# Performance work log

Hardware: AMD Instinct MI355X
Metric: run time of the kernel (lower is better)

The kernel has to match this reference:

```python
import jax, jax.numpy as jnp
import numpy as np

EMB = 1024
HEADS = 16
QKV = 64
INNER = 2816  # 256 * ceil(2*1024*4/3 / 256)


def rms_norm(x, w, eps=1e-6):
    xf = x.astype(jnp.float32)
    n = xf * jax.lax.rsqrt(jnp.mean(xf * xf, axis=-1, keepdims=True) + eps)
    return n.astype(x.dtype) * w


def setup_inputs() -> dict:
    key = jax.random.key(0)
    ks = jax.random.split(key, 12)
    s = 0.02
    return {
        "x": jax.random.normal(ks[0], (4, 2048, EMB), dtype=jnp.float32),
        "Wq": jax.random.normal(ks[1], (HEADS * QKV, EMB), dtype=jnp.float32) * s,
        "Wk": jax.random.normal(ks[2], (HEADS * QKV, EMB), dtype=jnp.float32) * s,
        "Wv": jax.random.normal(ks[3], (HEADS * QKV, EMB), dtype=jnp.float32) * s,
        "Wc": jax.random.normal(ks[4], (EMB, HEADS * QKV), dtype=jnp.float32) * s,
        "bc": jnp.zeros((EMB,), dtype=jnp.float32),
        "g1": jnp.ones((EMB,), dtype=jnp.float32),
        "g2": jnp.ones((EMB,), dtype=jnp.float32),
        "L1": jax.random.normal(ks[5], (INNER, EMB), dtype=jnp.float32) * s,
        "L2": jax.random.normal(ks[6], (INNER, EMB), dtype=jnp.float32) * s,
        "L3": jax.random.normal(ks[7], (EMB, INNER), dtype=jnp.float32) * s,
    }


def reference(x, Wq, Wk, Wv, Wc, bc, g1, g2, L1, L2, L3):
    B, N, D = x.shape
    # QKV projections (torch Linear: y = x @ W.T), split into heads: [B,H,N,dk]
    q = (x @ Wq.T).reshape(B, N, HEADS, QKV).transpose(0, 2, 1, 3)
    k = (x @ Wk.T).reshape(B, N, HEADS, QKV).transpose(0, 2, 1, 3)
    v = (x @ Wv.T).reshape(B, N, HEADS, QKV).transpose(0, 2, 1, 3)
    # attention: explicit score matrix [B,H,N,N]
    score = jnp.einsum("bhnd,bhmd->bhnm", q, k) / jnp.sqrt(jnp.float32(QKV))
    weights = jax.nn.softmax(score, axis=-1)
    out = jnp.einsum("bhnm,bhmd->bhnd", weights, v)
    out = out.transpose(0, 2, 1, 3).reshape(B, N, HEADS * QKV)
    mha = out @ Wc.T + bc
    h = rms_norm(x + mha, g1)
    # parallel gated MLP: silu(h@L1.T) * (h@L2.T) @ L3.T
    ff = (jax.nn.silu(h @ L1.T) * (h @ L2.T)) @ L3.T
    return rms_norm(h + ff, g2)
```

## Files before the change

### kernel.cpp

```cpp
#include <hip/hip_runtime.h>
#include <hip/hip_bf16.h>


#define EMB   1024
#define HEADS 16
#define DK    64
#define INNER 2816
#define BATCH 4
#define NTOK  2048
#define MROWS (BATCH * NTOK)

#define QSCALE 0.18033688011112042f

typedef short bf16x8 __attribute__((ext_vector_type(8)));
typedef short s16x4  __attribute__((ext_vector_type(4)));
typedef float f32x4  __attribute__((ext_vector_type(4)));

typedef const void __attribute__((address_space(1)))* gas_cvp;
typedef void       __attribute__((address_space(3)))* las_vp;

__device__ __forceinline__ short to_bf16(float f) {
  union { float f; unsigned u; } x; x.f = f;
  unsigned r = x.u + 0x7FFFu + ((x.u >> 16) & 1u);
  return (short)(r >> 16);
}

__device__ __forceinline__ unsigned cvt_pk_bf16(float a, float b) {
  unsigned r;
  asm("v_cvt_pk_bf16_f32 %0, %1, %2" : "=v"(r) : "v"(a), "v"(b));
  return r;
}

__device__ __forceinline__ void gld16(void* lds, const void* g) {
  __builtin_amdgcn_global_load_lds((gas_cvp)g, (las_vp)lds, 16, 0, 0);
}

__global__ __launch_bounds__(256, 4)
void cvtk(const float* __restrict__ s, short* __restrict__ d, int n4) {
  int i = blockIdx.x * 256 + threadIdx.x;
  if (i < n4) {
    float4 v = ((const float4*)s)[i];
    s16x4 o;
    o[0] = to_bf16(v.x); o[1] = to_bf16(v.y);
    o[2] = to_bf16(v.z); o[3] = to_bf16(v.w);
    ((s16x4*)d)[i] = o;
  }
}

__global__ __launch_bounds__(256, 4)
void cvt_inter(const float* __restrict__ L1, const float* __restrict__ L2,
               short* __restrict__ d) {
  int i = blockIdx.x * 256 + threadIdx.x;
  if (i >= INNER * 256) return;
  int row = i >> 8, c4 = i & 255;
  float4 v1 = ((const float4*)L1)[i];
  float4 v2 = ((const float4*)L2)[i];
  s16x4 o1, o2;
  o1[0]=to_bf16(v1.x); o1[1]=to_bf16(v1.y); o1[2]=to_bf16(v1.z); o1[3]=to_bf16(v1.w);
  o2[0]=to_bf16(v2.x); o2[1]=to_bf16(v2.y); o2[2]=to_bf16(v2.z); o2[3]=to_bf16(v2.w);
  ((s16x4*)d)[(size_t)(2 * row) * 256 + c4]     = o1;
  ((s16x4*)d)[(size_t)(2 * row + 1) * 256 + c4] = o2;
}

template<int MODE>
__global__ __launch_bounds__(256, 2)
void gemm_bt(const short* __restrict__ A, const short* __restrict__ Bw,
             int M, int N, int K,
             void* __restrict__ out0,
             const float* __restrict__ aux0, const float* __restrict__ aux1)
{
  __shared__ short At[128 * 64];
  __shared__ short Bt[128 * 64];
  const int t = threadIdx.x;
  const int lane = t & 63;
  const int l15 = lane & 15, lhi = lane >> 4;
  const int w  = t >> 6;
  const int wm = (w >> 1) << 6;
  const int wn = (w & 1) << 6;
  const int tilesN = N >> 7;
  const int m0 = (blockIdx.x / tilesN) << 7;
  const int n0 = (blockIdx.x % tilesN) << 7;

  const int r = t >> 3;
  const int p = t & 7;
  const int psrc = p ^ (r & 7);
  const short* Ag = A  + (size_t)(m0 + r) * K + psrc * 8;
  const short* Bg = Bw + (size_t)(n0 + r) * K + psrc * 8;

  f32x4 acc[4][4];
  const f32x4 fz = {0.f, 0.f, 0.f, 0.f};
#pragma unroll
  for (int i = 0; i < 4; i++)
#pragma unroll
    for (int j = 0; j < 4; j++) acc[i][j] = fz;

  int aoff[2][4], boff[2][4];
#pragma unroll
  for (int kk = 0; kk < 2; kk++)
#pragma unroll
    for (int mt = 0; mt < 4; mt++) {
      int ra = wm + mt * 16 + l15;
      aoff[kk][mt] = ra * 128 + ((kk * 64 + lhi * 16) ^ ((ra & 7) << 4));
      int rb = wn + mt * 16 + l15;
      boff[kk][mt] = rb * 128 + ((kk * 64 + lhi * 16) ^ ((rb & 7) << 4));
    }

  for (int k0 = 0; k0 < K; k0 += 64) {
#pragma unroll
    for (int i = 0; i < 4; i++) {
      gld16((char*)At + t * 16 + i * 4096, Ag + (size_t)i * 32 * K + k0);
      gld16((char*)Bt + t * 16 + i * 4096, Bg + (size_t)i * 32 * K + k0);
    }
    __syncthreads();
#pragma unroll
    for (int kk = 0; kk < 2; kk++) {
      bf16x8 a[4], b[4];
#pragma unroll
      for (int mt = 0; mt < 4; mt++)
        a[mt] = *(const bf16x8*)((const char*)At + aoff[kk][mt]);
#pragma unroll
      for (int nt = 0; nt < 4; nt++)
        b[nt] = *(const bf16x8*)((const char*)Bt + boff[kk][nt]);
#pragma unroll
      for (int mt = 0; mt < 4; mt++)
#pragma unroll
        for (int nt = 0; nt < 4; nt++)
          acc[mt][nt] = __builtin_amdgcn_mfma_f32_16x16x32_bf16(
              a[mt], b[nt], acc[mt][nt], 0, 0, 0);
    }
    __syncthreads();
  }

#pragma unroll
  for (int mt = 0; mt < 4; mt++) {
#pragma unroll
    for (int nt = 0; nt < 4; nt++) {
      const int mb = m0 + wm + mt * 16 + lhi * 4;
      const int n  = n0 + wn + nt * 16 + l15;
      if constexpr (MODE == 1) {
#pragma unroll
        for (int j = 0; j < 4; j++) {
          size_t idx = (size_t)(mb + j) * 1024 + n;
          ((float*)out0)[idx] = acc[mt][nt][j] + aux1[n] + aux0[idx];
        }
      } else {
#pragma unroll
        for (int j = 0; j < 4; j++) {
          size_t idx = (size_t)(mb + j) * 1024 + n;
          ((float*)out0)[idx] = acc[mt][nt][j] + aux0[idx];
        }
      }
    }
  }
}

#define G256_LDA(buf, mh) do {                                              \
  const char* _b = (const char*)&lds[buf][0][0] + (mh) * 8192;              \
  _Pragma("unroll") for (int mt = 0; mt < 4; mt++)                          \
    _Pragma("unroll") for (int kk = 0; kk < 2; kk++)                        \
      af[mt][kk] = *(const bf16x8*)(_b + aoff[mt][kk]);                     \
} while (0)

#define G256_LDB(buf, nh) do {                                              \
  const char* _b = (const char*)&lds[buf][1][0] + (nh) * 4096;              \
  _Pragma("unroll") for (int nt = 0; nt < 2; nt++)                          \
    _Pragma("unroll") for (int kk = 0; kk < 2; kk++)                        \
      bN[nh][nt][kk] = *(const bf16x8*)(_b + boff[nt][kk]);                 \
} while (0)

#define G256_MFQ(mh, nh) do {                                               \
  __builtin_amdgcn_s_setprio(1);                                            \
  _Pragma("unroll") for (int mt = 0; mt < 4; mt++)                          \
    _Pragma("unroll") for (int nt = 0; nt < 2; nt++)                        \
      _Pragma("unroll") for (int kk = 0; kk < 2; kk++)                      \
        acc[(mh)*4+mt][(nh)*2+nt] = __builtin_amdgcn_mfma_f32_16x16x32_bf16(\
            af[mt][kk], bN[nh][nt][kk], acc[(mh)*4+mt][(nh)*2+nt], 0, 0, 0);\
  __builtin_amdgcn_s_setprio(0);                                            \
} while (0)

#define G256_SYNC() do {                                                    \
  __builtin_amdgcn_s_barrier();                                             \
  asm volatile("s_waitcnt lgkmcnt(0)" ::: "memory");                        \
  __builtin_amdgcn_sched_barrier(0);                                        \
} while (0)

template<int MODE>
__global__ __launch_bounds__(512, 2)
void gemm256(const short* __restrict__ A, const short* __restrict__ Bw,
             int M, int N, int K,
             void* __restrict__ out0, void* __restrict__ out1,
             void* __restrict__ out2)
{
  __shared__ short lds[2][2][16384];
  const int t = threadIdx.x;
  const int lane = t & 63;
  const int l15 = lane & 15, lhi = lane >> 4;
  const int w = t >> 6;
  const int wr = w >> 2, wc = w & 3;

  const int chunk = gridDim.x >> 3;
  const int bid = blockIdx.x;
  const int wg = (bid & 7) * chunk + (bid >> 3);
  const int tilesM = M >> 8;
  const int m0 = (wg % tilesM) << 8;
  const int n0 = (wg / tilesM) << 8;

  const int r = t >> 3, p = t & 7;
  const int psrc = p ^ (r & 7);
  const short* Ag = A  + (size_t)(m0 + r) * K + psrc * 8;
  const short* Bg = Bw + (size_t)(n0 + r) * K + psrc * 8;
  const int NT = K >> 6;

  f32x4 acc[8][4];
  const f32x4 fz = {0.f, 0.f, 0.f, 0.f};
#pragma unroll
  for (int i = 0; i < 8; i++)
#pragma unroll
    for (int j = 0; j < 4; j++) acc[i][j] = fz;

  int aoff[4][2], boff[2][2];
#pragma unroll
  for (int mt = 0; mt < 4; mt++)
#pragma unroll
    for (int kk = 0; kk < 2; kk++)
      aoff[mt][kk] = (wr * 128 + mt * 16 + l15) * 128 +
                     ((kk * 64 + lhi * 16) ^ ((l15 & 7) << 4));
#pragma unroll
  for (int nt = 0; nt < 2; nt++)
#pragma unroll
    for (int kk = 0; kk < 2; kk++)
      boff[nt][kk] = (wc * 64 + nt * 16 + l15) * 128 +
                     ((kk * 64 + lhi * 16) ^ ((l15 & 7) << 4));

  bf16x8 af[4][2], bN[2][2][2];

  auto stg = [&](int buf, int kt, int hh) {
    const int sel = hh >> 1, hf = hh & 1;
    short* dst = &lds[buf][sel][hf * 8192] + t * 8;
    const short* src = (sel ? Bg : Ag) + (size_t)(hf * 128) * K + kt * 64;
    gld16(dst, src);
    gld16(dst + 4096, src + (size_t)64 * K);
  };

  stg(0, 0, 0); stg(0, 0, 1); stg(0, 0, 2); stg(0, 0, 3);
  stg(1, 1, 0);
  asm volatile("s_waitcnt vmcnt(2)" ::: "memory");
  __builtin_amdgcn_s_barrier();

  for (int i = 0; i < NT / 2; ++i) {
    const int T1 = 2 * i + 1, T2 = 2 * i + 2, T3 = 2 * i + 3;
    G256_LDA(0, 0); G256_LDB(0, 0);
    stg(1, T1, 1);
    G256_SYNC();
    G256_MFQ(0, 0);
    __builtin_amdgcn_s_barrier();
    G256_LDB(0, 1);
    stg(1, T1, 2);
    G256_SYNC();
    G256_MFQ(0, 1);
    __builtin_amdgcn_s_barrier();
    G256_LDA(0, 1);
    stg(1, T1, 3);
    G256_SYNC();
    G256_MFQ(1, 1);
    __builtin_amdgcn_s_barrier();
    if (T2 < NT) stg(0, T2, 0);
    G256_SYNC();
    G256_MFQ(1, 0);
    if (T2 < NT) asm volatile("s_waitcnt vmcnt(2)" ::: "memory");
    else         asm volatile("s_waitcnt vmcnt(0)" ::: "memory");
    __builtin_amdgcn_s_barrier();
    G256_LDA(1, 0); G256_LDB(1, 0);
    if (T2 < NT) stg(0, T2, 1);
    G256_SYNC();
    G256_MFQ(0, 0);
    __builtin_amdgcn_s_barrier();
    G256_LDB(1, 1);
    if (T2 < NT) stg(0, T2, 2);
    G256_SYNC();
    G256_MFQ(0, 1);
    __builtin_amdgcn_s_barrier();
    G256_LDA(1, 1);
    if (T2 < NT) stg(0, T2, 3);
    G256_SYNC();
    G256_MFQ(1, 1);
    __builtin_amdgcn_s_barrier();
    if (T3 < NT) stg(1, T3, 0);
    G256_SYNC();
    G256_MFQ(1, 0);
    if (T3 < NT) asm volatile("s_waitcnt vmcnt(2)" ::: "memory");
    else         asm volatile("s_waitcnt vmcnt(0)" ::: "memory");
    __builtin_amdgcn_s_barrier();
  }

#pragma unroll
  for (int mt = 0; mt < 8; mt++) {
#pragma unroll
    for (int nt = 0; nt < 4; nt++) {
      const int mb = m0 + wr * 128 + mt * 16 + lhi * 4;
      const int n  = n0 + wc * 64 + nt * 16 + l15;
      if constexpr (MODE == 0) {
        const int which = n >> 10, c = n & 1023;
        if (which == 2) {
          const int hh = c >> 6, dd = c & 63;
          const int bb = mb >> 11, tok = mb & 2047;
          s16x4 pk;
#pragma unroll
          for (int j = 0; j < 4; j++) pk[j] = to_bf16(acc[mt][nt][j]);
          *(s16x4*)((short*)out2 +
                    (size_t)((bb * HEADS + hh) * DK + dd) * NTOK + tok) = pk;
        } else {
          short* dst = (which == 0) ? (short*)out0 : (short*)out1;
          const float scl = (which == 0) ? QSCALE : 1.0f;
#pragma unroll
          for (int j = 0; j < 4; j++)
            dst[(size_t)(mb + j) * 1024 + c] = to_bf16(acc[mt][nt][j] * scl);
        }
      } else {
#pragma unroll
        for (int j = 0; j < 4; j++) {
          float v0 = acc[mt][nt][j];
          float v1 = __shfl_xor(v0, 1);
          if ((lane & 1) == 0) {
            float su = v0 / (1.f + __expf(-v0));
            ((short*)out0)[(size_t)(mb + j) * INNER + (n >> 1)] =
                to_bf16(su * v1);
          }
        }
      }
    }
  }
}

__global__ __launch_bounds__(256, 3)
void attn_k(const short* __restrict__ qb, const short* __restrict__ kb,
            const short* __restrict__ vtb, short* __restrict__ ob)
{
  __shared__ short Kt[2][64 * 64];
  __shared__ short Vt[2][64 * 64];
  __shared__ short Pt[128 * 68];
  const int t = threadIdx.x;
  const int lane = t & 63;
  const int l15 = lane & 15, lhi = lane >> 4;
  const int w = t >> 6;
  const int bh = blockIdx.x;
  const int b = bh >> 4, h = bh & 15;
  const int q0 = blockIdx.y << 7;

  bf16x8 aq[2][2];
#pragma unroll
  for (int s = 0; s < 2; s++) {
    const short* qp = qb + (size_t)(b * NTOK + q0 + w * 32 + s * 16 + l15) * EMB
                         + h * DK + lhi * 8;
    aq[s][0] = *(const bf16x8*)qp;
    aq[s][1] = *(const bf16x8*)(qp + 32);
  }

  f32x4 acc[2][4];
  const f32x4 fz = {0.f, 0.f, 0.f, 0.f};
#pragma unroll
  for (int s = 0; s < 2; s++)
#pragma unroll
    for (int dt = 0; dt < 4; dt++) acc[s][dt] = fz;
  float m_run[2] = {-1e30f, -1e30f};
  float l_run[2] = {0.f, 0.f};

  const int r = t >> 3, p = t & 7;
  const int psrc = p ^ (r & 7);
  const short* kg = kb  + (size_t)(b * NTOK + r) * EMB + h * DK + psrc * 8;
  const short* vg = vtb + (size_t)(bh * DK + r) * NTOK + psrc * 8;

  int kvoff[4][2];
#pragma unroll
  for (int x = 0; x < 4; x++)
#pragma unroll
    for (int kk = 0; kk < 2; kk++) {
      int row = x * 16 + l15;
      kvoff[x][kk] = row * 128 + ((kk * 64 + lhi * 16) ^ ((row & 7) << 4));
    }
  int pw[2][4], pr[2][2];
#pragma unroll
  for (int s = 0; s < 2; s++) {
    const int prow = w * 32 + s * 16 + l15;
#pragma unroll
    for (int kvt = 0; kvt < 4; kvt++) pw[s][kvt] = prow * 136 + kvt * 32 + lhi * 8;
#pragma unroll
    for (int kk = 0; kk < 2; kk++)   pr[s][kk]  = prow * 136 + kk * 64 + lhi * 16;
  }

  auto stage = [&](short* Kd, short* Vd, int kv0) {
    const short* ks = kg + (size_t)kv0 * EMB;
    const short* vs = vg + kv0;
    gld16(Kd + t * 8,        ks);
    gld16(Kd + t * 8 + 2048, ks + (size_t)32 * EMB);
    gld16(Vd + t * 8,        vs);
    gld16(Vd + t * 8 + 2048, vs + (size_t)32 * NTOK);
  };

  auto do_set = [&](f32x4 (&sv)[4], float& mr, float& lr, f32x4 (&ac)[4],
                    const int (&pwo)[4]) {
    float pm = sv[0][0];
#pragma unroll
    for (int kvt = 0; kvt < 4; kvt++)
#pragma unroll
      for (int j = 0; j < 4; j++) pm = fmaxf(pm, sv[kvt][j]);
    if (__any(pm > mr + 8.0f)) {
      pm = fmaxf(pm, __shfl_xor(pm, 16));
      pm = fmaxf(pm, __shfl_xor(pm, 32));
      const float mnew = fmaxf(mr, pm);
      const float al = exp2f(mr - mnew);
      lr *= al;
#pragma unroll
      for (int dt = 0; dt < 4; dt++)
#pragma unroll
        for (int j = 0; j < 4; j++) ac[dt][j] *= al;
      mr = mnew;
    }
    float ls = 0.f;
#pragma unroll
    for (int kvt = 0; kvt < 4; kvt++)
#pragma unroll
      for (int j = 0; j < 4; j++) {
        float pe = exp2f(sv[kvt][j] - mr);
        sv[kvt][j] = pe;
        ls += pe;
      }
    lr += ls;
#pragma unroll
    for (int kvt = 0; kvt < 4; kvt++) {
      uint2 u;
      u.x = cvt_pk_bf16(sv[kvt][0], sv[kvt][1]);
      u.y = cvt_pk_bf16(sv[kvt][2], sv[kvt][3]);
      *(uint2*)((char*)Pt + pwo[kvt]) = u;
    }
  };

  auto compute = [&](const short* Kb_, const short* Vb_) {
    const char* Kb = (const char*)Kb_;
    const char* Vb = (const char*)Vb_;
    bf16x8 kf[4][2];
#pragma unroll
    for (int x = 0; x < 4; x++)
#pragma unroll
      for (int kk = 0; kk < 2; kk++)
        kf[x][kk] = *(const bf16x8*)(Kb + kvoff[x][kk]);
    f32x4 s0[4], s1[4];
    __builtin_amdgcn_s_setprio(1);
#pragma unroll
    for (int kvt = 0; kvt < 4; kvt++) {
      s0[kvt] = __builtin_amdgcn_mfma_f32_16x16x32_bf16(kf[kvt][0], aq[0][0], fz, 0, 0, 0);
      s0[kvt] = __builtin_amdgcn_mfma_f32_16x16x32_bf16(kf[kvt][1], aq[0][1], s0[kvt], 0, 0, 0);
      s1[kvt] = __builtin_amdgcn_mfma_f32_16x16x32_bf16(kf[kvt][0], aq[1][0], fz, 0, 0, 0);
      s1[kvt] = __builtin_amdgcn_mfma_f32_16x16x32_bf16(kf[kvt][1], aq[1][1], s1[kvt], 0, 0, 0);
    }
    __builtin_amdgcn_s_setprio(0);
    do_set(s0, m_run[0], l_run[0], acc[0], pw[0]);
    do_set(s1, m_run[1], l_run[1], acc[1], pw[1]);
    bf16x8 vf[4][2];
#pragma unroll
    for (int dt = 0; dt < 4; dt++)
#pragma unroll
      for (int kk = 0; kk < 2; kk++)
        vf[dt][kk] = *(const bf16x8*)(Vb + kvoff[dt][kk]);
    bf16x8 pb0[2], pb1[2];
#pragma unroll
    for (int kk = 0; kk < 2; kk++) {
      pb0[kk] = *(const bf16x8*)((const char*)Pt + pr[0][kk]);
      pb1[kk] = *(const bf16x8*)((const char*)Pt + pr[1][kk]);
    }
    __builtin_amdgcn_s_setprio(1);
#pragma unroll
    for (int dt = 0; dt < 4; dt++) {
#pragma unroll
      for (int kk = 0; kk < 2; kk++)
        acc[0][dt] = __builtin_amdgcn_mfma_f32_16x16x32_bf16(vf[dt][kk], pb0[kk], acc[0][dt], 0, 0, 0);
#pragma unroll
      for (int kk = 0; kk < 2; kk++)
        acc[1][dt] = __builtin_amdgcn_mfma_f32_16x16x32_bf16(vf[dt][kk], pb1[kk], acc[1][dt], 0, 0, 0);
    }
    __builtin_amdgcn_s_setprio(0);
  };

  stage(Kt[0], Vt[0], 0);
  for (int it = 0; it < 32; it += 2) {
    stage(Kt[1], Vt[1], (it + 1) * 64);
    asm volatile("s_waitcnt vmcnt(4)" ::: "memory");
    __builtin_amdgcn_s_barrier();
    compute(Kt[0], Vt[0]);
    __builtin_amdgcn_s_barrier();
    if (it + 2 < 32) {
      stage(Kt[0], Vt[0], (it + 2) * 64);
      asm volatile("s_waitcnt vmcnt(4)" ::: "memory");
    } else {
      asm volatile("s_waitcnt vmcnt(0)" ::: "memory");
    }
    __builtin_amdgcn_s_barrier();
    compute(Kt[1], Vt[1]);
    __builtin_amdgcn_s_barrier();
  }

#pragma unroll
  for (int s = 0; s < 2; s++) {
    float lt = l_run[s];
    lt += __shfl_xor(lt, 16);
    lt += __shfl_xor(lt, 32);
    const float inv = 1.f / lt;
    short* op = ob + (size_t)(b * NTOK + q0 + w * 32 + s * 16 + l15) * EMB + h * DK;
#pragma unroll
    for (int dt = 0; dt < 4; dt++) {
      s16x4 pk;
#pragma unroll
      for (int j = 0; j < 4; j++) pk[j] = to_bf16(acc[s][dt][j] * inv);
      *(s16x4*)(op + dt * 16 + lhi * 4) = pk;
    }
  }
}

template<bool WB>
__global__ __launch_bounds__(256, 4)
void rmsnorm_k(const float* __restrict__ in, const float* __restrict__ gw,
               float* __restrict__ of, short* __restrict__ ob)
{
  const int row = blockIdx.x;
  const int t = threadIdx.x;
  const float4 v = ((const float4*)(in + (size_t)row * EMB))[t];
  float ss = v.x * v.x + v.y * v.y + v.z * v.z + v.w * v.w;
#pragma unroll
  for (int off = 1; off < 64; off <<= 1) ss += __shfl_xor(ss, off);
  __shared__ float red[4];
  if ((t & 63) == 0) red[t >> 6] = ss;
  __syncthreads();
  float tot = red[0] + red[1] + red[2] + red[3];
  const float rinv = rsqrtf(tot * (1.f / EMB) + 1e-6f);
  const float4 g4 = ((const float4*)gw)[t];
  float4 o;
  o.x = v.x * rinv * g4.x; o.y = v.y * rinv * g4.y;
  o.z = v.z * rinv * g4.z; o.w = v.w * rinv * g4.w;
  ((float4*)(of + (size_t)row * EMB))[t] = o;
  if (WB) {
    s16x4 pk;
    pk[0] = to_bf16(o.x); pk[1] = to_bf16(o.y);
    pk[2] = to_bf16(o.z); pk[3] = to_bf16(o.w);
    ((s16x4*)(ob + (size_t)row * EMB))[t] = pk;
  }
}

extern "C" void kernel_launch(void* const* d_in, const int* in_sizes, int n_in,
                              void* d_out, int out_size, void* d_ws, size_t ws_size,
                              hipStream_t stream)
{
  const float* x  = (const float*)d_in[0];
  const float* Wq = (const float*)d_in[1];
  const float* Wk = (const float*)d_in[2];
  const float* Wv = (const float*)d_in[3];
  const float* Wc = (const float*)d_in[4];
  const float* bc = (const float*)d_in[5];
  const float* g1 = (const float*)d_in[6];
  const float* g2 = (const float*)d_in[7];
  const float* L1 = (const float*)d_in[8];
  const float* L2 = (const float*)d_in[9];
  const float* L3 = (const float*)d_in[10];
  float* out = (float*)d_out;

  char* ws = (char*)d_ws;
  size_t o = 0;
  auto take = [&](size_t bytes) -> char* {
    char* pp = ws + o;
    o += (bytes + 255) & ~(size_t)255;
    return pp;
  };
  short* xb   = (short*)take((size_t)MROWS * EMB * 2);
  short* wqkv = (short*)take((size_t)3072 * 1024 * 2);
  short* wcb  = (short*)take((size_t)1024 * 1024 * 2);
  short* l12  = (short*)take((size_t)5632 * 1024 * 2);
  short* l3b  = (short*)take((size_t)1024 * 2816 * 2);
  short* q    = (short*)take((size_t)MROWS * EMB * 2);
  short* k    = (short*)take((size_t)MROWS * EMB * 2);
  short* v    = (short*)take((size_t)MROWS * EMB * 2);
  short* attn = (short*)take((size_t)MROWS * EMB * 2);
  float* t1   = (float*)take((size_t)MROWS * EMB * 4);
  float* h32  = (float*)take((size_t)MROWS * EMB * 4);
  short* hb   = (short*)take((size_t)MROWS * EMB * 2);
  short* gated = q;
  float* t2    = t1;

  cvtk<<<MROWS * EMB / 4 / 256, 256, 0, stream>>>(x, xb, MROWS * EMB / 4);
  cvtk<<<1024 * 1024 / 4 / 256, 256, 0, stream>>>(Wq, wqkv, 1024 * 1024 / 4);
  cvtk<<<1024 * 1024 / 4 / 256, 256, 0, stream>>>(Wk, wqkv + 1024 * 1024, 1024 * 1024 / 4);
  cvtk<<<1024 * 1024 / 4 / 256, 256, 0, stream>>>(Wv, wqkv + 2 * 1024 * 1024, 1024 * 1024 / 4);
  cvtk<<<1024 * 1024 / 4 / 256, 256, 0, stream>>>(Wc, wcb, 1024 * 1024 / 4);
  cvt_inter<<<INNER, 256, 0, stream>>>(L1, L2, l12);
  cvtk<<<1024 * 2816 / 4 / 256, 256, 0, stream>>>(L3, l3b, 1024 * 2816 / 4);

  gemm256<0><<<32 * 12, 512, 0, stream>>>(xb, wqkv, MROWS, 3072, 1024,
                                          q, k, v);
  attn_k<<<dim3(64, 16), 256, 0, stream>>>(q, k, v, attn);
  gemm_bt<1><<<64 * 8, 256, 0, stream>>>(attn, wcb, MROWS, 1024, 1024,
                                         t1, x, bc);
  rmsnorm_k<true><<<MROWS, 256, 0, stream>>>(t1, g1, h32, hb);
  gemm256<2><<<32 * 22, 512, 0, stream>>>(hb, l12, MROWS, 5632, 1024,
                                          gated, nullptr, nullptr);
  gemm_bt<3><<<64 * 8, 256, 0, stream>>>(gated, l3b, MROWS, 1024, 2816,
                                         t2, h32, nullptr);
  rmsnorm_k<false><<<MROWS, 256, 0, stream>>>(t2, g2, out, nullptr);
}
```

Baseline: 462.3 us.

## Remap warp tiles to LDS halves and deepen global-load prefetch in gemm256

Changes the warp-to-output mapping so each wave's M and N subtiles fall in separate 128-row halves of the staged tile, matching the half-tile LDS stage granularity. The prefetch schedule is reordered so loads run further ahead, with finer vmcnt waits that only need the half currently being consumed, and the final K iteration is peeled into an epilogue. The intent is to hide global-load latency better and cut stalls at barriers. It relies on precise vmcnt counting, and a miscounted wait would silently read stale LDS data.

```diff
diff --git a/kernel.cpp b/kernel.cpp
--- a/kernel.cpp
+++ b/kernel.cpp
@@ -155,14 +155,14 @@
 }
 
 #define G256_LDA(buf, mh) do {                                              \
-  const char* _b = (const char*)&lds[buf][0][0] + (mh) * 8192;              \
+  const char* _b = (const char*)&lds[buf][0][0] + (mh) * 16384;             \
   _Pragma("unroll") for (int mt = 0; mt < 4; mt++)                          \
     _Pragma("unroll") for (int kk = 0; kk < 2; kk++)                        \
       af[mt][kk] = *(const bf16x8*)(_b + aoff[mt][kk]);                     \
 } while (0)
 
 #define G256_LDB(buf, nh) do {                                              \
-  const char* _b = (const char*)&lds[buf][1][0] + (nh) * 4096;              \
+  const char* _b = (const char*)&lds[buf][1][0] + (nh) * 16384;             \
   _Pragma("unroll") for (int nt = 0; nt < 2; nt++)                          \
     _Pragma("unroll") for (int kk = 0; kk < 2; kk++)                        \
       bN[nh][nt][kk] = *(const bf16x8*)(_b + boff[nt][kk]);                 \
@@ -183,6 +183,8 @@
   asm volatile("s_waitcnt lgkmcnt(0)" ::: "memory");                        \
   __builtin_amdgcn_sched_barrier(0);                                        \
 } while (0)
+
+#define G256_WAIT(n) asm volatile("s_waitcnt vmcnt(" #n ")" ::: "memory")
 
 template<int MODE>
 __global__ __launch_bounds__(512, 2)
@@ -223,13 +225,13 @@
   for (int mt = 0; mt < 4; mt++)
 #pragma unroll
     for (int kk = 0; kk < 2; kk++)
-      aoff[mt][kk] = (wr * 128 + mt * 16 + l15) * 128 +
+      aoff[mt][kk] = (wr * 64 + mt * 16 + l15) * 128 +
                      ((kk * 64 + lhi * 16) ^ ((l15 & 7) << 4));
 #pragma unroll
   for (int nt = 0; nt < 2; nt++)
 #pragma unroll
     for (int kk = 0; kk < 2; kk++)
-      boff[nt][kk] = (wc * 64 + nt * 16 + l15) * 128 +
+      boff[nt][kk] = (wc * 32 + nt * 16 + l15) * 128 +
                      ((kk * 64 + lhi * 16) ^ ((l15 & 7) << 4));
 
   bf16x8 af[4][2], bN[2][2][2];
@@ -242,63 +244,104 @@
     gld16(dst + 4096, src + (size_t)64 * K);
   };
 
-  stg(0, 0, 0); stg(0, 0, 1); stg(0, 0, 2); stg(0, 0, 3);
-  stg(1, 1, 0);
-  asm volatile("s_waitcnt vmcnt(2)" ::: "memory");
+  stg(0, 0, 0); stg(0, 0, 2); stg(0, 0, 3); stg(0, 0, 1);
+  stg(1, 1, 0); stg(1, 1, 2); stg(1, 1, 3);
+  G256_WAIT(10);
   __builtin_amdgcn_s_barrier();
 
-  for (int i = 0; i < NT / 2; ++i) {
-    const int T1 = 2 * i + 1, T2 = 2 * i + 2, T3 = 2 * i + 3;
+  for (int i = 0; i < NT / 2 - 1; ++i) {
+    const int Ta = 2 * i + 1, Tb = 2 * i + 2, Tc = 2 * i + 3;
     G256_LDA(0, 0); G256_LDB(0, 0);
-    stg(1, T1, 1);
+    stg(1, Ta, 1);
     G256_SYNC();
     G256_MFQ(0, 0);
+    G256_WAIT(10);
     __builtin_amdgcn_s_barrier();
     G256_LDB(0, 1);
-    stg(1, T1, 2);
+    stg(0, Tb, 0);
     G256_SYNC();
     G256_MFQ(0, 1);
+    G256_WAIT(10);
     __builtin_amdgcn_s_barrier();
     G256_LDA(0, 1);
-    stg(1, T1, 3);
+    stg(0, Tb, 2);
     G256_SYNC();
     G256_MFQ(1, 1);
     __builtin_amdgcn_s_barrier();
-    if (T2 < NT) stg(0, T2, 0);
+    stg(0, Tb, 3);
     G256_SYNC();
     G256_MFQ(1, 0);
-    if (T2 < NT) asm volatile("s_waitcnt vmcnt(2)" ::: "memory");
-    else         asm volatile("s_waitcnt vmcnt(0)" ::: "memory");
+    G256_WAIT(10);
     __builtin_amdgcn_s_barrier();
     G256_LDA(1, 0); G256_LDB(1, 0);
-    if (T2 < NT) stg(0, T2, 1);
+    stg(0, Tb, 1);
     G256_SYNC();
     G256_MFQ(0, 0);
+    G256_WAIT(10);
     __builtin_amdgcn_s_barrier();
     G256_LDB(1, 1);
-    if (T2 < NT) stg(0, T2, 2);
+    stg(1, Tc, 0);
     G256_SYNC();
     G256_MFQ(0, 1);
+    G256_WAIT(10);
     __builtin_amdgcn_s_barrier();
     G256_LDA(1, 1);
-    if (T2 < NT) stg(0, T2, 3);
+    stg(1, Tc, 2);
     G256_SYNC();
     G256_MFQ(1, 1);
     __builtin_amdgcn_s_barrier();
-    if (T3 < NT) stg(1, T3, 0);
+    stg(1, Tc, 3);
     G256_SYNC();
     G256_MFQ(1, 0);
-    if (T3 < NT) asm volatile("s_waitcnt vmcnt(2)" ::: "memory");
-    else         asm volatile("s_waitcnt vmcnt(0)" ::: "memory");
-    __builtin_amdgcn_s_barrier();
+    G256_WAIT(10);
+    __builtin_amdgcn_s_barrier();
+  }
+
+  {
+    const int Ta = NT - 1;
+    G256_LDA(0, 0); G256_LDB(0, 0);
+    stg(1, Ta, 1);
+    G256_SYNC();
+    G256_MFQ(0, 0);
+    G256_WAIT(10);
+    __builtin_amdgcn_s_barrier();
+    G256_LDB(0, 1);
+    G256_SYNC();
+    G256_MFQ(0, 1);
+    G256_WAIT(8);
+    __builtin_amdgcn_s_barrier();
+    G256_LDA(0, 1);
+    G256_SYNC();
+    G256_MFQ(1, 1);
+    __builtin_amdgcn_s_barrier();
+    G256_SYNC();
+    G256_MFQ(1, 0);
+    G256_WAIT(4);
+    __builtin_amdgcn_s_barrier();
+    G256_LDA(1, 0); G256_LDB(1, 0);
+    G256_SYNC();
+    G256_MFQ(0, 0);
+    G256_WAIT(2);
+    __builtin_amdgcn_s_barrier();
+    G256_LDB(1, 1);
+    G256_SYNC();
+    G256_MFQ(0, 1);
+    G256_WAIT(0);
+    __builtin_amdgcn_s_barrier();
+    G256_LDA(1, 1);
+    G256_SYNC();
+    G256_MFQ(1, 1);
+    __builtin_amdgcn_s_barrier();
+    G256_SYNC();
+    G256_MFQ(1, 0);
   }
 
 #pragma unroll
   for (int mt = 0; mt < 8; mt++) {
 #pragma unroll
     for (int nt = 0; nt < 4; nt++) {
-      const int mb = m0 + wr * 128 + mt * 16 + lhi * 4;
-      const int n  = n0 + wc * 64 + nt * 16 + l15;
+      const int mb = m0 + (mt >> 2) * 128 + wr * 64 + (mt & 3) * 16 + lhi * 4;
+      const int n  = n0 + (nt >> 1) * 128 + wc * 32 + (nt & 1) * 16 + l15;
       if constexpr (MODE == 0) {
         const int which = n >> 10, c = n & 1023;
         if (which == 2) {
```

Measured after the change: 460.1 us. About the same (-0.5%).
